# Kernel optimization log

Measured on AMD Instinct MI355X. Metric: run time of the kernel, lower is better.

The kernel has to match this reference:

```python
import jax, jax.numpy as jnp
import numpy as np

N, E = 20000, 100000
D_IN, H1, C1 = 512, 8, 64   # conv1: 512 -> 8 heads x 64, concat -> 512
H2, C2 = 4, 128             # conv2: 512 -> 4 heads x 128, mean -> 128


def setup_inputs() -> dict:
    key = jax.random.key(0)
    k = jax.random.split(key, 12)
    s_in = 1.0 / np.sqrt(D_IN).astype(np.float32)
    return {
        "street_embedding": jax.random.normal(k[0], (N, D_IN), jnp.float32),
        "edge_index": jax.random.randint(k[1], (2, E), 0, N),
        "y": jax.random.randint(k[2], (N,), 0, C2),
        "train_mask": jax.random.bernoulli(k[3], 0.5, (N,)),
        "W1": jax.random.normal(k[4], (D_IN, H1 * C1), jnp.float32) * s_in,
        "att_src1": jax.random.normal(k[5], (H1, C1), jnp.float32) * 0.1,
        "att_dst1": jax.random.normal(k[6], (H1, C1), jnp.float32) * 0.1,
        "b1": jnp.zeros((H1 * C1,), jnp.float32),
        "W2": jax.random.normal(k[7], (H1 * C1, H2 * C2), jnp.float32) * s_in,
        "att_src2": jax.random.normal(k[8], (H2, C2), jnp.float32) * 0.1,
        "att_dst2": jax.random.normal(k[9], (H2, C2), jnp.float32) * 0.1,
        "b2": jnp.zeros((C2,), jnp.float32),
    }


def _gat_conv(x, W, a_src, a_dst, b, src, dst, n, H, C, concat):
    # linear transform (no bias, as in PyG GATConv's internal lin)
    xp = (x @ W).reshape(n, H, C)                      # [N,H,C]
    asrc = jnp.einsum('nhc,hc->nh', xp, a_src)         # [N,H]
    adst = jnp.einsum('nhc,hc->nh', xp, a_dst)
    e = jax.nn.leaky_relu(asrc[src] + adst[dst], 0.2)  # [E',H] edge scores
    # softmax over incoming edges per destination node
    m = jax.lax.stop_gradient(jax.ops.segment_max(e, dst, num_segments=n))
    ex = jnp.exp(e - m[dst])
    denom = jax.ops.segment_sum(ex, dst, num_segments=n)
    alpha = ex / (denom[dst] + 1e-16)                  # [E',H]
    out = jax.ops.segment_sum(alpha[:, :, None] * xp[src], dst, num_segments=n)  # [N,H,C]
    if concat:
        return out.reshape(n, H * C) + b
    return out.mean(axis=1) + b


def reference(street_embedding, edge_index, y, train_mask,
              W1, att_src1, att_dst1, b1, W2, att_src2, att_dst2, b2):
    n = street_embedding.shape[0]
    loop = jnp.arange(n)
    # PyG GATConv adds self-loops by default
    src = jnp.concatenate([edge_index[0], loop])
    dst = jnp.concatenate([edge_index[1], loop])
    # dropout layers are identity in eval mode
    h = _gat_conv(street_embedding, W1, att_src1, att_dst1, b1, src, dst, n, H1, C1, True)
    h = jax.nn.elu(h)
    out = _gat_conv(h, W2, att_src2, att_dst2, b2, src, dst, n, H2, C2, False)  # [N,C2]
    # CrossEntropyLoss, mean over train_mask nodes (weighted mean, jit-safe)
    logp = jax.nn.log_softmax(out, axis=-1)
    ce = -jnp.take_along_axis(logp, y[:, None], axis=-1)[:, 0]
    w = train_mask.astype(out.dtype)
    loss_su = jnp.sum(w * ce) / jnp.sum(w)
    return (loss_su, out)
```

## Files before the change

### kernel.cpp

```cpp
#include <hip/hip_runtime.h>
#include <cmath>

#define D_IN 512
#define HC   512
#define NH1  8
#define NC1  64
#define NH2  4
#define NC2  128
#define BM 128
#define BN 128
#define BK 64

typedef __attribute__((ext_vector_type(8))) short short8;
typedef __attribute__((ext_vector_type(8))) unsigned short u16x8;
typedef __attribute__((ext_vector_type(4))) float f32x4;

__device__ inline ushort f2bf(float f) {
  unsigned u = __float_as_uint(f);
  return (ushort)((u + 0x7FFFu + ((u >> 16) & 1u)) >> 16);
}
__device__ inline float bf2f(ushort b) { return __uint_as_float(((unsigned)b) << 16); }

__global__ void k_pre(const float* __restrict__ x, ushort* __restrict__ Abf,
                      const float* __restrict__ W1, const float* __restrict__ W2,
                      ushort* __restrict__ Wt1, ushort* __restrict__ Wt2, int n4x,
                      const int* __restrict__ ei, int E, int Etot,
                      int* __restrict__ cnt) {
  const int KN = D_IN * HC;
  int i = blockIdx.x * blockDim.x + threadIdx.x;
  if (i < n4x) {
    float4 v = ((const float4*)x)[i];
    ushort4 r = { f2bf(v.x), f2bf(v.y), f2bf(v.z), f2bf(v.w) };
    ((ushort4*)Abf)[i] = r;
  } else if (i < n4x + 2 * KN) {
    int idx = i - n4x;
    const float* W = (idx < KN) ? W1 : W2;
    ushort* Wt = (idx < KN) ? Wt1 : Wt2;
    int j = (idx < KN) ? idx : idx - KN;
    int n = j / D_IN, k = j - n * D_IN;
    Wt[j] = f2bf(W[(size_t)k * HC + n]);
  } else {
    int e = i - n4x - 2 * KN;
    if (e >= Etot) return;
    int d = (e < E) ? ei[E + e] : e - E;
    atomicAdd(&cnt[d], 1);
  }
}

template<int H>
__global__ void k_gemm_bf16(const ushort* __restrict__ A, const ushort* __restrict__ Bt,
                            ushort* __restrict__ Cbf,
                            const float* __restrict__ att_s, const float* __restrict__ att_d,
                            float* __restrict__ asrc, float* __restrict__ adst, int M) {
  constexpr int C = HC / H;
  __shared__ __align__(16) ushort As[BM * BK];
  __shared__ __align__(16) ushort Bs[BN * BK];
  int t = threadIdx.x;
  int m0 = blockIdx.y * BM;
  int n0 = blockIdx.x * BN;
  int wave = t >> 6, lane = t & 63;
  int ln = lane & 15, qd = lane >> 4;
  int wm = (wave >> 1) * 64, wn = (wave & 1) * 64;

  f32x4 acc[4][4] = {};

  int g = t >> 6, ct = (t >> 4) & 3, lt = t & 15;
  int rA0 = m0 + g * 16 + lt;      if (rA0 > M - 1) rA0 = M - 1;
  int rA1 = m0 + 64 + g * 16 + lt; if (rA1 > M - 1) rA1 = M - 1;
  const ushort* gA0 = A + (size_t)rA0 * D_IN + ct * 8;
  const ushort* gA1 = A + (size_t)rA1 * D_IN + ct * 8;
  const ushort* gB0 = Bt + (size_t)(n0 + g * 16 + lt) * D_IN + ct * 8;
  const ushort* gB1 = Bt + (size_t)(n0 + 64 + g * 16 + lt) * D_IN + ct * 8;

  for (int k0 = 0; k0 < D_IN; k0 += BK) {
    __syncthreads();
#pragma unroll
    for (int h = 0; h < 2; ++h) {
      int ko = k0 + h * 32;
      int lo = h * 4096;
      __builtin_amdgcn_global_load_lds(
          (const __attribute__((address_space(1))) void*)(gA0 + ko),
          (__attribute__((address_space(3))) void*)(As + lo + t * 8), 16, 0, 0);
      __builtin_amdgcn_global_load_lds(
          (const __attribute__((address_space(1))) void*)(gA1 + ko),
          (__attribute__((address_space(3))) void*)(As + lo + 2048 + t * 8), 16, 0, 0);
      __builtin_amdgcn_global_load_lds(
          (const __attribute__((address_space(1))) void*)(gB0 + ko),
          (__attribute__((address_space(3))) void*)(Bs + lo + t * 8), 16, 0, 0);
      __builtin_amdgcn_global_load_lds(
          (const __attribute__((address_space(1))) void*)(gB1 + ko),
          (__attribute__((address_space(3))) void*)(Bs + lo + 2048 + t * 8), 16, 0, 0);
    }
    __syncthreads();
#pragma unroll
    for (int h = 0; h < 2; ++h) {
      int lo = h * 4096;
      short8 a[4], bb[4];
#pragma unroll
      for (int i = 0; i < 4; ++i)
        a[i] = *(const short8*)&As[lo + (((wave >> 1) * 4 + i) * 4 + qd) * 128 + ln * 8];
#pragma unroll
      for (int j = 0; j < 4; ++j)
        bb[j] = *(const short8*)&Bs[lo + (((wave & 1) * 4 + j) * 4 + qd) * 128 + ln * 8];
#pragma unroll
      for (int i = 0; i < 4; ++i)
#pragma unroll
        for (int j = 0; j < 4; ++j)
          acc[i][j] = __builtin_amdgcn_mfma_f32_16x16x32_bf16(a[i], bb[j], acc[i][j], 0, 0, 0);
    }
  }

#pragma unroll
  for (int i = 0; i < 4; ++i) {
#pragma unroll
    for (int reg = 0; reg < 4; ++reg) {
      int row = m0 + wm + i * 16 + qd * 4 + reg;
      if (row >= M) continue;
#pragma unroll
      for (int j = 0; j < 4; ++j)
        Cbf[(size_t)row * HC + n0 + wn + j * 16 + ln] = f2bf(acc[i][j][reg]);
    }
  }

  int colbase = n0 + wn;
  int h = colbase / C;
  float sa[4], da[4];
#pragma unroll
  for (int j = 0; j < 4; ++j) {
    int c = (colbase % C) + j * 16 + ln;
    sa[j] = att_s[h * C + c];
    da[j] = att_d[h * C + c];
  }
#pragma unroll
  for (int i = 0; i < 4; ++i) {
#pragma unroll
    for (int reg = 0; reg < 4; ++reg) {
      float ps = acc[i][0][reg] * sa[0] + acc[i][1][reg] * sa[1]
               + acc[i][2][reg] * sa[2] + acc[i][3][reg] * sa[3];
      float pd = acc[i][0][reg] * da[0] + acc[i][1][reg] * da[1]
               + acc[i][2][reg] * da[2] + acc[i][3][reg] * da[3];
#pragma unroll
      for (int o = 1; o < 16; o <<= 1) { ps += __shfl_xor(ps, o); pd += __shfl_xor(pd, o); }
      int row = m0 + wm + i * 16 + qd * 4 + reg;
      if (ln == 0 && row < M) {
        if (C == 64) {
          asrc[row * H + h] = ps; adst[row * H + h] = pd;
        } else {
          int sub = (colbase >> 6) & 1;
          asrc[(row * H + h) * 2 + sub] = ps;
          adst[(row * H + h) * 2 + sub] = pd;
        }
      }
    }
  }
}

__global__ void k_scan(const int* __restrict__ cnt, int* __restrict__ rowstart, int N) {
  int tid = threadIdx.x;
  int T = (N + 1023) / 1024;
  int base = tid * T;
  int sum = 0;
  for (int i = 0; i < T; ++i) { int j = base + i; if (j < N) sum += cnt[j]; }
  int lane = tid & 63, w = tid >> 6;
  int v = sum;
#pragma unroll
  for (int off = 1; off < 64; off <<= 1) {
    int u = __shfl_up(v, off);
    if (lane >= off) v += u;
  }
  __shared__ int wsum[16];
  if (lane == 63) wsum[w] = v;
  __syncthreads();
  if (tid < 16) {
    int tv = wsum[tid];
#pragma unroll
    for (int off = 1; off < 16; off <<= 1) {
      int u = __shfl_up(tv, off);
      if (tid >= off) tv += u;
    }
    wsum[tid] = tv;
  }
  __syncthreads();
  int wave_prefix = (w == 0) ? 0 : wsum[w - 1];
  int run = wave_prefix + v - sum;
  for (int i = 0; i < T; ++i) {
    int j = base + i;
    if (j < N) { rowstart[j] = run; run += cnt[j]; }
  }
  if (tid == 1023) rowstart[N] = run;
}

__global__ void k_scatter(const int* __restrict__ ei, int E, int Etot,
                          const int* __restrict__ rowstart, int* __restrict__ cursor,
                          int* __restrict__ csr_src) {
  int e = blockIdx.x * blockDim.x + threadIdx.x;
  if (e >= Etot) return;
  int s = (e < E) ? ei[e] : e - E;
  int d = (e < E) ? ei[E + e] : e - E;
  int pos = atomicAdd(&cursor[d], 1);
  csr_src[rowstart[d] + pos] = s;
}

__global__ void k_agg1(const int* __restrict__ rowstart, const int* __restrict__ csr_src,
                       const float* __restrict__ asrc, const float* __restrict__ adst,
                       const ushort* __restrict__ xp, ushort* __restrict__ hout,
                       const float* __restrict__ bias, int N) {
  int wv = threadIdx.x >> 6, lane = threadIdx.x & 63;
  int s = blockIdx.x & 7;
  int n = (blockIdx.x >> 3) * 4 + wv;
  if (n >= N) return;
  int beg = rowstart[n], end = rowstart[n + 1];
  float adn = adst[n * NH1 + s];
  const ushort* xs = xp + (size_t)s * NC1 + lane;

  float accv = 0.f, wsum = 0.f;
  for (int c0 = beg; c0 < end; c0 += 64) {
    int len = end - c0; if (len > 64) len = 64;
    int ev = (lane < len) ? csr_src[c0 + lane] : 0;
    int j = 0;
    for (; j + 1 < len; j += 2) {
      int s0 = __shfl(ev, j), s1 = __shfl(ev, j + 1);
      float v0 = asrc[s0 * NH1 + s] + adn;
      float v1 = asrc[s1 * NH1 + s] + adn;
      ushort x0 = xs[(size_t)s0 * HC];
      ushort x1 = xs[(size_t)s1 * HC];
      v0 = (v0 > 0.f) ? v0 : 0.2f * v0;
      v1 = (v1 > 0.f) ? v1 : 0.2f * v1;
      float w0 = __expf(v0), w1 = __expf(v1);
      accv += w0 * bf2f(x0) + w1 * bf2f(x1);
      wsum += w0 + w1;
    }
    if (j < len) {
      int s0 = __shfl(ev, j);
      float v0 = asrc[s0 * NH1 + s] + adn;
      ushort x0 = xs[(size_t)s0 * HC];
      v0 = (v0 > 0.f) ? v0 : 0.2f * v0;
      float w0 = __expf(v0);
      accv += w0 * bf2f(x0);
      wsum += w0;
    }
  }
  float v = accv / (wsum + 1e-16f) + bias[s * NC1 + lane];
  v = (v > 0.f) ? v : expm1f(v);
  hout[(size_t)n * HC + s * NC1 + lane] = f2bf(v);
}

__global__ void k_agg2(const int* __restrict__ rowstart, const int* __restrict__ csr_src,
                       const float* __restrict__ asrc, const float* __restrict__ adst,
                       const ushort* __restrict__ xp,
                       float* __restrict__ out2, const float* __restrict__ bias,
                       const int* __restrict__ y, const int* __restrict__ msk,
                       float* __restrict__ acc2, int N) {
  constexpr int H = NH2;
  int wv = threadIdx.x >> 6, lane = threadIdx.x & 63;
  int n = blockIdx.x * 4 + wv;
  if (n >= N) return;
  int h = lane >> 4;
  int beg = rowstart[n], end = rowstart[n + 1];

  float2 t2 = ((const float2*)adst)[n * H + h];
  float adn = t2.x + t2.y;

  float acc[8] = {};
  float wsum = 0.f;

  for (int c0 = beg; c0 < end; c0 += 64) {
    int len = end - c0; if (len > 64) len = 64;
    int ev = (lane < len) ? csr_src[c0 + lane] : 0;
    int j = 0;
    for (; j + 1 < len; j += 2) {
      int s0 = __shfl(ev, j), s1 = __shfl(ev, j + 1);
      float2 p0 = ((const float2*)asrc)[s0 * H + h];
      float2 p1 = ((const float2*)asrc)[s1 * H + h];
      float v0 = p0.x + p0.y + adn;
      float v1 = p1.x + p1.y + adn;
      u16x8 a0 = ((const u16x8*)xp)[(size_t)s0 * 64 + lane];
      u16x8 a1 = ((const u16x8*)xp)[(size_t)s1 * 64 + lane];
      v0 = (v0 > 0.f) ? v0 : 0.2f * v0;
      v1 = (v1 > 0.f) ? v1 : 0.2f * v1;
      float w0 = __expf(v0), w1 = __expf(v1);
#pragma unroll
      for (int k = 0; k < 8; ++k)
        acc[k] += w0 * bf2f(a0[k]) + w1 * bf2f(a1[k]);
      wsum += w0 + w1;
    }
    if (j < len) {
      int s0 = __shfl(ev, j);
      float2 p0 = ((const float2*)asrc)[s0 * H + h];
      float v0 = p0.x + p0.y + adn;
      u16x8 a0 = ((const u16x8*)xp)[(size_t)s0 * 64 + lane];
      v0 = (v0 > 0.f) ? v0 : 0.2f * v0;
      float w0 = __expf(v0);
#pragma unroll
      for (int k = 0; k < 8; ++k) acc[k] += w0 * bf2f(a0[k]);
      wsum += w0;
    }
  }
  float rdn = 1.0f / (wsum + 1e-16f);
#pragma unroll
  for (int k = 0; k < 8; ++k) acc[k] *= rdn;

#pragma unroll
  for (int k = 0; k < 8; ++k) {
    float v = acc[k];
    v += __shfl_xor(v, 16);
    v += __shfl_xor(v, 32);
    acc[k] = v * 0.25f + bias[(lane & 15) * 8 + k];
  }
  if (lane < 16) {
    int cb = lane * 8;
#pragma unroll
    for (int k = 0; k < 8; ++k) out2[(size_t)n * NC2 + cb + k] = acc[k];
  }
  float mx = acc[0];
#pragma unroll
  for (int k = 1; k < 8; ++k) mx = fmaxf(mx, acc[k]);
#pragma unroll
  for (int o = 1; o < 16; o <<= 1) mx = fmaxf(mx, __shfl_xor(mx, o));
  float e = 0.f;
#pragma unroll
  for (int k = 0; k < 8; ++k) e += __expf(acc[k] - mx);
#pragma unroll
  for (int o = 1; o < 16; o <<= 1) e += __shfl_xor(e, o);
  int yv = y[n];
  float sel = acc[0];
#pragma unroll
  for (int k = 1; k < 8; ++k) sel = ((yv & 7) == k) ? acc[k] : sel;
  float vy = __shfl(sel, yv >> 3);
  if (lane == 0 && msk[n] != 0) {
    float ce = mx + logf(e) - vy;
    int slot = n & 127;
    atomicAdd(&acc2[slot], ce);
    atomicAdd(&acc2[128 + slot], 1.0f);
  }
}

__global__ void k_final(const float* __restrict__ acc2, float* __restrict__ out0) {
  int tid = threadIdx.x;
  float ce = acc2[tid], ct = acc2[128 + tid];
#pragma unroll
  for (int o = 32; o > 0; o >>= 1) { ce += __shfl_xor(ce, o); ct += __shfl_xor(ct, o); }
  __shared__ float s[4];
  if ((tid & 63) == 0) { s[(tid >> 6) * 2] = ce; s[(tid >> 6) * 2 + 1] = ct; }
  __syncthreads();
  if (tid == 0) out0[0] = (s[0] + s[2]) / (s[1] + s[3]);
}

extern "C" void kernel_launch(void* const* d_in, const int* in_sizes, int n_in,
                              void* d_out, int out_size, void* d_ws, size_t ws_size,
                              hipStream_t stream) {
  const float* x   = (const float*)d_in[0];
  const int*   ei  = (const int*)d_in[1];
  const int*   y   = (const int*)d_in[2];
  const int*   msk = (const int*)d_in[3];
  const float* W1  = (const float*)d_in[4];
  const float* as1 = (const float*)d_in[5];
  const float* ad1 = (const float*)d_in[6];
  const float* b1  = (const float*)d_in[7];
  const float* W2  = (const float*)d_in[8];
  const float* as2 = (const float*)d_in[9];
  const float* ad2 = (const float*)d_in[10];
  const float* b2  = (const float*)d_in[11];
  float* out = (float*)d_out;

  int N = in_sizes[0] / D_IN;
  int E = in_sizes[1] / 2;
  int Etot = E + N;

  float* ws = (float*)d_ws;
  size_t NF = (size_t)N * HC;
  float* asr1 = ws;
  float* adt1 = asr1 + (size_t)N * NH1;
  float* asr2 = adt1 + (size_t)N * NH1;
  float* adt2 = asr2 + (size_t)N * 2 * NH2;
  float* acc2 = adt2 + (size_t)N * 2 * NH2;
  int*   cnt    = (int*)(acc2 + 256);
  int*   cursor = cnt + N;
  size_t zero_bytes = (256 + 2 * (size_t)N) * sizeof(float);
  int*   rowstart = cursor + N;
  int*   csr_src  = rowstart + N + 1;
  ushort* xpbf = (ushort*)((((uintptr_t)(csr_src + Etot)) + 15) & ~(uintptr_t)15);
  ushort* Abf = xpbf + NF;
  ushort* Wt1 = Abf + NF;
  ushort* Wt2 = Wt1 + (size_t)D_IN * HC;

  hipMemsetAsync(acc2, 0, zero_bytes, stream);

  int n4x = (int)(NF / 4);
  int pre_total = n4x + 2 * D_IN * HC + Etot;
  k_pre<<<(pre_total + 255) / 256, 256, 0, stream>>>(x, Abf, W1, W2, Wt1, Wt2, n4x,
                                                     ei, E, Etot, cnt);

  k_scan<<<1, 1024, 0, stream>>>(cnt, rowstart, N);
  k_scatter<<<(Etot + 255) / 256, 256, 0, stream>>>(ei, E, Etot, rowstart, cursor, csr_src);

  dim3 ggrid(HC / BN, (N + BM - 1) / BM);
  int agg1blocks = 8 * ((N + 3) / 4);
  int agg2blocks = (N + 3) / 4;

  k_gemm_bf16<NH1><<<ggrid, 256, 0, stream>>>(Abf, Wt1, xpbf, as1, ad1, asr1, adt1, N);
  k_agg1<<<agg1blocks, 256, 0, stream>>>(rowstart, csr_src, asr1, adt1, xpbf, Abf, b1, N);

  k_gemm_bf16<NH2><<<ggrid, 256, 0, stream>>>(Abf, Wt2, xpbf, as2, ad2, asr2, adt2, N);
  k_agg2<<<agg2blocks, 256, 0, stream>>>(rowstart, csr_src, asr2, adt2, xpbf,
                                         out + 1, b2, y, msk, acc2, N);

  k_final<<<1, 128, 0, stream>>>(acc2, out);
}
```

Before: 330.3 us.

## Fold scan into GEMM, XCD-aware tile order, unified wide-vector aggregation kernels

The separate prefix-scan kernel is removed and its work is done by one extra workgroup of the first GEMM launch. GEMM tiles are remapped with an XCD-aware swizzle so neighbouring tiles land on the same chiplet's L2. Layer-1 aggregation now handles all 8 heads per wave using 16-byte vector loads of 8 bf16 values per lane, replacing 8 blocks per node that each did 2-byte loads. A shared templated kernel also unrolls the edge loop by 4 to keep more gathers in flight. The risks are higher register pressure, and the scan workgroup running longer than an average GEMM tile.

```diff
diff --git a/kernel.cpp b/kernel.cpp
--- a/kernel.cpp
+++ b/kernel.cpp
@@ -47,17 +47,51 @@
   }
 }
 
-template<int H>
+template<int H, int SCAN>
 __global__ void k_gemm_bf16(const ushort* __restrict__ A, const ushort* __restrict__ Bt,
                             ushort* __restrict__ Cbf,
                             const float* __restrict__ att_s, const float* __restrict__ att_d,
-                            float* __restrict__ asrc, float* __restrict__ adst, int M) {
+                            float* __restrict__ asrc, float* __restrict__ adst, int M,
+                            const int* __restrict__ cnt, int* __restrict__ rowstart, int Nn) {
   constexpr int C = HC / H;
   __shared__ __align__(16) ushort As[BM * BK];
   __shared__ __align__(16) ushort Bs[BN * BK];
   int t = threadIdx.x;
-  int m0 = blockIdx.y * BM;
-  int n0 = blockIdx.x * BN;
+
+  if (SCAN && blockIdx.x == 0) {
+    __shared__ int wsum[4];
+    int T = (Nn + 255) / 256;
+    int base = t * T;
+    int sum = 0;
+    for (int i = 0; i < T; ++i) { int j = base + i; if (j < Nn) sum += cnt[j]; }
+    int lane = t & 63, w = t >> 6;
+    int v = sum;
+#pragma unroll
+    for (int off = 1; off < 64; off <<= 1) {
+      int u = __shfl_up(v, off);
+      if (lane >= off) v += u;
+    }
+    if (lane == 63) wsum[w] = v;
+    __syncthreads();
+    int wp = 0;
+    for (int i = 0; i < w; ++i) wp += wsum[i];
+    int run = wp + v - sum;
+    for (int i = 0; i < T; ++i) {
+      int j = base + i;
+      if (j < Nn) { rowstart[j] = run; run += cnt[j]; }
+    }
+    if (t == 255) rowstart[Nn] = run;
+    return;
+  }
+
+  int lin = blockIdx.x - (SCAN ? 1 : 0);
+  int nwg = gridDim.x - (SCAN ? 1 : 0);
+  int q = nwg >> 3, r = nwg & 7;
+  int xcd = lin & 7, pos = lin >> 3;
+  int wg = (xcd < r ? xcd * (q + 1) : r * (q + 1) + (xcd - r) * q) + pos;
+  int m0 = (wg >> 2) * BM;
+  int n0 = (wg & 3) * BN;
+
   int wave = t >> 6, lane = t & 63;
   int ln = lane & 15, qd = lane >> 4;
   int wm = (wave >> 1) * 64, wn = (wave & 1) * 64;
@@ -155,41 +189,6 @@
   }
 }
 
-__global__ void k_scan(const int* __restrict__ cnt, int* __restrict__ rowstart, int N) {
-  int tid = threadIdx.x;
-  int T = (N + 1023) / 1024;
-  int base = tid * T;
-  int sum = 0;
-  for (int i = 0; i < T; ++i) { int j = base + i; if (j < N) sum += cnt[j]; }
-  int lane = tid & 63, w = tid >> 6;
-  int v = sum;
-#pragma unroll
-  for (int off = 1; off < 64; off <<= 1) {
-    int u = __shfl_up(v, off);
-    if (lane >= off) v += u;
-  }
-  __shared__ int wsum[16];
-  if (lane == 63) wsum[w] = v;
-  __syncthreads();
-  if (tid < 16) {
-    int tv = wsum[tid];
-#pragma unroll
-    for (int off = 1; off < 16; off <<= 1) {
-      int u = __shfl_up(tv, off);
-      if (tid >= off) tv += u;
-    }
-    wsum[tid] = tv;
-  }
-  __syncthreads();
-  int wave_prefix = (w == 0) ? 0 : wsum[w - 1];
-  int run = wave_prefix + v - sum;
-  for (int i = 0; i < T; ++i) {
-    int j = base + i;
-    if (j < N) { rowstart[j] = run; run += cnt[j]; }
-  }
-  if (tid == 1023) rowstart[N] = run;
-}
-
 __global__ void k_scatter(const int* __restrict__ ei, int E, int Etot,
                           const int* __restrict__ rowstart, int* __restrict__ cursor,
                           int* __restrict__ csr_src) {
@@ -201,137 +200,121 @@
   csr_src[rowstart[d] + pos] = s;
 }
 
-__global__ void k_agg1(const int* __restrict__ rowstart, const int* __restrict__ csr_src,
-                       const float* __restrict__ asrc, const float* __restrict__ adst,
-                       const ushort* __restrict__ xp, ushort* __restrict__ hout,
-                       const float* __restrict__ bias, int N) {
+template<int H, int MODE>
+__global__ void k_agg(const int* __restrict__ rowstart, const int* __restrict__ csr_src,
+                      const float* __restrict__ asrc, const float* __restrict__ adst,
+                      const ushort* __restrict__ xp, ushort* __restrict__ hout,
+                      float* __restrict__ out2, const float* __restrict__ bias,
+                      const int* __restrict__ y, const int* __restrict__ msk,
+                      float* __restrict__ acc2, int N) {
   int wv = threadIdx.x >> 6, lane = threadIdx.x & 63;
-  int s = blockIdx.x & 7;
-  int n = (blockIdx.x >> 3) * 4 + wv;
+  int n = blockIdx.x * 4 + wv;
   if (n >= N) return;
+  int h = (MODE == 1) ? (lane >> 3) : (lane >> 4);
   int beg = rowstart[n], end = rowstart[n + 1];
-  float adn = adst[n * NH1 + s];
-  const ushort* xs = xp + (size_t)s * NC1 + lane;
-
-  float accv = 0.f, wsum = 0.f;
+
+  float adn;
+  if (MODE == 1) adn = adst[n * H + h];
+  else { float2 t2 = ((const float2*)adst)[n * H + h]; adn = t2.x + t2.y; }
+
+  float acc[8] = {};
+  float wsum = 0.f;
+
+#define SCR(s_)  ((MODE == 1) ? asrc[(s_) * H + h] \
+                   : (((const float2*)asrc)[(s_) * H + h].x + \
+                      ((const float2*)asrc)[(s_) * H + h].y))
+#define EDGE(w_, a_)  do {                                   \
+    float ww = (w_);                                         \
+    _Pragma("unroll") for (int k = 0; k < 8; ++k)            \
+      acc[k] += ww * bf2f((a_)[k]);                          \
+    wsum += ww; } while (0)
+#define LRELU(v_) ((v_) > 0.f ? (v_) : 0.2f * (v_))
+
   for (int c0 = beg; c0 < end; c0 += 64) {
     int len = end - c0; if (len > 64) len = 64;
     int ev = (lane < len) ? csr_src[c0 + lane] : 0;
     int j = 0;
+    for (; j + 3 < len; j += 4) {
+      int s0 = __shfl(ev, j), s1 = __shfl(ev, j + 1);
+      int s2 = __shfl(ev, j + 2), s3 = __shfl(ev, j + 3);
+      float v0 = SCR(s0) + adn, v1 = SCR(s1) + adn;
+      float v2 = SCR(s2) + adn, v3 = SCR(s3) + adn;
+      u16x8 a0 = ((const u16x8*)xp)[(size_t)s0 * 64 + lane];
+      u16x8 a1 = ((const u16x8*)xp)[(size_t)s1 * 64 + lane];
+      u16x8 a2 = ((const u16x8*)xp)[(size_t)s2 * 64 + lane];
+      u16x8 a3 = ((const u16x8*)xp)[(size_t)s3 * 64 + lane];
+      EDGE(__expf(LRELU(v0)), a0);
+      EDGE(__expf(LRELU(v1)), a1);
+      EDGE(__expf(LRELU(v2)), a2);
+      EDGE(__expf(LRELU(v3)), a3);
+    }
     for (; j + 1 < len; j += 2) {
       int s0 = __shfl(ev, j), s1 = __shfl(ev, j + 1);
-      float v0 = asrc[s0 * NH1 + s] + adn;
-      float v1 = asrc[s1 * NH1 + s] + adn;
-      ushort x0 = xs[(size_t)s0 * HC];
-      ushort x1 = xs[(size_t)s1 * HC];
-      v0 = (v0 > 0.f) ? v0 : 0.2f * v0;
-      v1 = (v1 > 0.f) ? v1 : 0.2f * v1;
-      float w0 = __expf(v0), w1 = __expf(v1);
-      accv += w0 * bf2f(x0) + w1 * bf2f(x1);
-      wsum += w0 + w1;
+      float v0 = SCR(s0) + adn, v1 = SCR(s1) + adn;
+      u16x8 a0 = ((const u16x8*)xp)[(size_t)s0 * 64 + lane];
+      u16x8 a1 = ((const u16x8*)xp)[(size_t)s1 * 64 + lane];
+      EDGE(__expf(LRELU(v0)), a0);
+      EDGE(__expf(LRELU(v1)), a1);
     }
     if (j < len) {
       int s0 = __shfl(ev, j);
-      float v0 = asrc[s0 * NH1 + s] + adn;
-      ushort x0 = xs[(size_t)s0 * HC];
-      v0 = (v0 > 0.f) ? v0 : 0.2f * v0;
-      float w0 = __expf(v0);
-      accv += w0 * bf2f(x0);
-      wsum += w0;
-    }
-  }
-  float v = accv / (wsum + 1e-16f) + bias[s * NC1 + lane];
-  v = (v > 0.f) ? v : expm1f(v);
-  hout[(size_t)n * HC + s * NC1 + lane] = f2bf(v);
-}
-
-__global__ void k_agg2(const int* __restrict__ rowstart, const int* __restrict__ csr_src,
-                       const float* __restrict__ asrc, const float* __restrict__ adst,
-                       const ushort* __restrict__ xp,
-                       float* __restrict__ out2, const float* __restrict__ bias,
-                       const int* __restrict__ y, const int* __restrict__ msk,
-                       float* __restrict__ acc2, int N) {
-  constexpr int H = NH2;
-  int wv = threadIdx.x >> 6, lane = threadIdx.x & 63;
-  int n = blockIdx.x * 4 + wv;
-  if (n >= N) return;
-  int h = lane >> 4;
-  int beg = rowstart[n], end = rowstart[n + 1];
-
-  float2 t2 = ((const float2*)adst)[n * H + h];
-  float adn = t2.x + t2.y;
-
-  float acc[8] = {};
-  float wsum = 0.f;
-
-  for (int c0 = beg; c0 < end; c0 += 64) {
-    int len = end - c0; if (len > 64) len = 64;
-    int ev = (lane < len) ? csr_src[c0 + lane] : 0;
-    int j = 0;
-    for (; j + 1 < len; j += 2) {
-      int s0 = __shfl(ev, j), s1 = __shfl(ev, j + 1);
-      float2 p0 = ((const float2*)asrc)[s0 * H + h];
-      float2 p1 = ((const float2*)asrc)[s1 * H + h];
-      float v0 = p0.x + p0.y + adn;
-      float v1 = p1.x + p1.y + adn;
+      float v0 = SCR(s0) + adn;
       u16x8 a0 = ((const u16x8*)xp)[(size_t)s0 * 64 + lane];
-      u16x8 a1 = ((const u16x8*)xp)[(size_t)s1 * 64 + lane];
-      v0 = (v0 > 0.f) ? v0 : 0.2f * v0;
-      v1 = (v1 > 0.f) ? v1 : 0.2f * v1;
-      float w0 = __expf(v0), w1 = __expf(v1);
-#pragma unroll
-      for (int k = 0; k < 8; ++k)
-        acc[k] += w0 * bf2f(a0[k]) + w1 * bf2f(a1[k]);
-      wsum += w0 + w1;
-    }
-    if (j < len) {
-      int s0 = __shfl(ev, j);
-      float2 p0 = ((const float2*)asrc)[s0 * H + h];
-      float v0 = p0.x + p0.y + adn;
-      u16x8 a0 = ((const u16x8*)xp)[(size_t)s0 * 64 + lane];
-      v0 = (v0 > 0.f) ? v0 : 0.2f * v0;
-      float w0 = __expf(v0);
-#pragma unroll
-      for (int k = 0; k < 8; ++k) acc[k] += w0 * bf2f(a0[k]);
-      wsum += w0;
-    }
-  }
+      EDGE(__expf(LRELU(v0)), a0);
+    }
+  }
+#undef SCR
+#undef EDGE
+#undef LRELU
+
   float rdn = 1.0f / (wsum + 1e-16f);
 #pragma unroll
   for (int k = 0; k < 8; ++k) acc[k] *= rdn;
 
-#pragma unroll
-  for (int k = 0; k < 8; ++k) {
-    float v = acc[k];
-    v += __shfl_xor(v, 16);
-    v += __shfl_xor(v, 32);
-    acc[k] = v * 0.25f + bias[(lane & 15) * 8 + k];
-  }
-  if (lane < 16) {
-    int cb = lane * 8;
-#pragma unroll
-    for (int k = 0; k < 8; ++k) out2[(size_t)n * NC2 + cb + k] = acc[k];
-  }
-  float mx = acc[0];
-#pragma unroll
-  for (int k = 1; k < 8; ++k) mx = fmaxf(mx, acc[k]);
-#pragma unroll
-  for (int o = 1; o < 16; o <<= 1) mx = fmaxf(mx, __shfl_xor(mx, o));
-  float e = 0.f;
-#pragma unroll
-  for (int k = 0; k < 8; ++k) e += __expf(acc[k] - mx);
-#pragma unroll
-  for (int o = 1; o < 16; o <<= 1) e += __shfl_xor(e, o);
-  int yv = y[n];
-  float sel = acc[0];
-#pragma unroll
-  for (int k = 1; k < 8; ++k) sel = ((yv & 7) == k) ? acc[k] : sel;
-  float vy = __shfl(sel, yv >> 3);
-  if (lane == 0 && msk[n] != 0) {
-    float ce = mx + logf(e) - vy;
-    int slot = n & 127;
-    atomicAdd(&acc2[slot], ce);
-    atomicAdd(&acc2[128 + slot], 1.0f);
+  if (MODE == 1) {
+    int c = lane * 8;
+    u16x8 rr;
+#pragma unroll
+    for (int k = 0; k < 8; ++k) {
+      float v = acc[k] + bias[c + k];
+      v = (v > 0.f) ? v : expm1f(v);
+      rr[k] = f2bf(v);
+    }
+    ((u16x8*)hout)[(size_t)n * 64 + lane] = rr;
+  } else {
+#pragma unroll
+    for (int k = 0; k < 8; ++k) {
+      float v = acc[k];
+      v += __shfl_xor(v, 16);
+      v += __shfl_xor(v, 32);
+      acc[k] = v * 0.25f + bias[(lane & 15) * 8 + k];
+    }
+    if (lane < 16) {
+      int cb = lane * 8;
+#pragma unroll
+      for (int k = 0; k < 8; ++k) out2[(size_t)n * NC2 + cb + k] = acc[k];
+    }
+    float mx = acc[0];
+#pragma unroll
+    for (int k = 1; k < 8; ++k) mx = fmaxf(mx, acc[k]);
+#pragma unroll
+    for (int o = 1; o < 16; o <<= 1) mx = fmaxf(mx, __shfl_xor(mx, o));
+    float e = 0.f;
+#pragma unroll
+    for (int k = 0; k < 8; ++k) e += __expf(acc[k] - mx);
+#pragma unroll
+    for (int o = 1; o < 16; o <<= 1) e += __shfl_xor(e, o);
+    int yv = y[n];
+    float sel = acc[0];
+#pragma unroll
+    for (int k = 1; k < 8; ++k) sel = ((yv & 7) == k) ? acc[k] : sel;
+    float vy = __shfl(sel, yv >> 3);
+    if (lane == 0 && msk[n] != 0) {
+      float ce = mx + logf(e) - vy;
+      int slot = n & 127;
+      atomicAdd(&acc2[slot], ce);
+      atomicAdd(&acc2[128 + slot], 1.0f);
+    }
   }
 }
 
@@ -391,19 +374,19 @@
   k_pre<<<(pre_total + 255) / 256, 256, 0, stream>>>(x, Abf, W1, W2, Wt1, Wt2, n4x,
                                                      ei, E, Etot, cnt);
 
-  k_scan<<<1, 1024, 0, stream>>>(cnt, rowstart, N);
+  int nwg = (HC / BN) * ((N + BM - 1) / BM);
+  int aggblocks = (N + 3) / 4;
+
+  k_gemm_bf16<NH1, 1><<<nwg + 1, 256, 0, stream>>>(Abf, Wt1, xpbf, as1, ad1, asr1, adt1, N,
+                                                   cnt, rowstart, N);
   k_scatter<<<(Etot + 255) / 256, 256, 0, stream>>>(ei, E, Etot, rowstart, cursor, csr_src);
-
-  dim3 ggrid(HC / BN, (N + BM - 1) / BM);
-  int agg1blocks = 8 * ((N + 3) / 4);
-  int agg2blocks = (N + 3) / 4;
-
-  k_gemm_bf16<NH1><<<ggrid, 256, 0, stream>>>(Abf, Wt1, xpbf, as1, ad1, asr1, adt1, N);
-  k_agg1<<<agg1blocks, 256, 0, stream>>>(rowstart, csr_src, asr1, adt1, xpbf, Abf, b1, N);
-
-  k_gemm_bf16<NH2><<<ggrid, 256, 0, stream>>>(Abf, Wt2, xpbf, as2, ad2, asr2, adt2, N);
-  k_agg2<<<agg2blocks, 256, 0, stream>>>(rowstart, csr_src, asr2, adt2, xpbf,
-                                         out + 1, b2, y, msk, acc2, N);
+  k_agg<NH1, 1><<<aggblocks, 256, 0, stream>>>(rowstart, csr_src, asr1, adt1, xpbf, Abf,
+                                               nullptr, b1, nullptr, nullptr, nullptr, N);
+
+  k_gemm_bf16<NH2, 0><<<nwg, 256, 0, stream>>>(Abf, Wt2, xpbf, as2, ad2, asr2, adt2, N,
+                                               nullptr, nullptr, N);
+  k_agg<NH2, 2><<<aggblocks, 256, 0, stream>>>(rowstart, csr_src, asr2, adt2, xpbf, nullptr,
+                                               out + 1, b2, y, msk, acc2, N);
 
   k_final<<<1, 128, 0, stream>>>(acc2, out);
 }
```

Result: faster. 292.6 us (-11.4%).
